# Optimization experiments

Hardware: AMD Instinct MI355X
Metric: run time of the kernel (lower is better)

## Reference

```python
import jax, jax.numpy as jnp
import numpy as np

NUM_EXPERT = 16
IN_FEAT = 1024
OUT_FEAT = 1024
BATCH = 8192


def setup_inputs() -> dict:
    key = jax.random.key(0)
    k_inp, k_gate, k_w = jax.random.split(key, 3)
    inp = jax.random.normal(k_inp, (BATCH, IN_FEAT), dtype=jnp.float32)
    gate = jax.random.randint(k_gate, (BATCH,), 0, NUM_EXPERT, dtype=jnp.int32)
    # nn.Linear default init: uniform(-1/sqrt(in_feat), 1/sqrt(in_feat))
    bound = 1.0 / np.sqrt(IN_FEAT)
    weight = jax.random.uniform(
        k_w, (NUM_EXPERT, OUT_FEAT, IN_FEAT), dtype=jnp.float32,
        minval=-bound, maxval=bound)
    return {"inp": inp, "gate": gate, "weight": weight}


def reference(inp, gate, weight):
    # o[t] = weight[gate[t]] @ inp[t]
    # Loop over the (small, fixed) expert axis via lax.scan; each step does a
    # dense [B, in] @ [in, out] GEMM and keeps rows routed to that expert.
    num_expert, out_feat, _ = weight.shape
    batch = inp.shape[0]

    def body(o, xs):
        i, w = xs  # w: [out_feat, in_feat]
        y = inp @ w.T  # [batch, out_feat]
        sel = (gate == i)[:, None]
        return jnp.where(sel, y, o), None

    o0 = jnp.zeros((batch, out_feat), dtype=inp.dtype)
    o, _ = jax.lax.scan(body, o0, (jnp.arange(num_expert), weight))
    return o
```

## Files before the change

### kernel.cpp

```cpp
#include <hip/hip_runtime.h>
#include <hip/hip_bf16.h>

#define NE    16
#define KDIM  1024
#define NDIM  1024
#define BATCH 8192
#define TM    128
#define TN    64
#define MAXT  96

typedef __attribute__((ext_vector_type(8))) short short8;
typedef __attribute__((ext_vector_type(4))) float floatx4;
typedef unsigned short ushort_t;

#define O_CNT  0
#define O_TG0  256
#define O_TE   1024
#define O_TEND 2048
#define O_POS  4096
#define O_TOK  36864
#define O_PA   73728
#define WS_REQ 17113088

#define GLOAD_LDS(gp, lp) __builtin_amdgcn_global_load_lds( \
    (const __attribute__((address_space(1))) unsigned int*)(gp), \
    (__attribute__((address_space(3))) unsigned int*)(lp), 16, 0, 0)

__device__ __forceinline__ unsigned int pk2bf(float x, float y) {
    __hip_bfloat162 h = __float22bfloat162_rn(make_float2(x, y));
    unsigned int u;
    __builtin_memcpy(&u, &h, 4);
    return u;
}


__global__ void zero_k(int* cnt) {
    if (threadIdx.x < NE) cnt[threadIdx.x] = 0;
}

__global__ void hist_k(const int* __restrict__ gate, int* cnt, int* pos) {
    int t = blockIdx.x * blockDim.x + threadIdx.x;
    if (t < BATCH) pos[t] = atomicAdd(&cnt[gate[t]], 1);
}

__global__ __launch_bounds__(256, 8) void prep_k(
        const float* __restrict__ inp, const int* __restrict__ gate,
        const int* __restrict__ pos, const int* __restrict__ cnt,
        ushort_t* __restrict__ pA, int* __restrict__ tok,
        int* __restrict__ tg0, int* __restrict__ te, int* __restrict__ tend) {
    __shared__ int ntot;
    const int b = blockIdx.x, tid = threadIdx.x;
    if (b < 2048) {
        const int col = (tid & 127) * 8;
        const int half = tid >> 7;
        int g[2]; float4 v0[2], v1[2];
        #pragma unroll
        for (int p = 0; p < 2; ++p) {
            int t = b * 4 + p * 2 + half;
            int e = gate[t];
            int off = 0;
            #pragma unroll
            for (int k = 0; k < NE; ++k) off += (k < e) ? cnt[k] : 0;
            g[p] = off + pos[t];
            v0[p] = *(const float4*)&inp[(size_t)t * KDIM + col];
            v1[p] = *(const float4*)&inp[(size_t)t * KDIM + col + 4];
        }
        #pragma unroll
        for (int p = 0; p < 2; ++p) {
            uint4 u = make_uint4(pk2bf(v0[p].x, v0[p].y), pk2bf(v0[p].z, v0[p].w),
                                 pk2bf(v1[p].x, v1[p].y), pk2bf(v1[p].z, v1[p].w));
            *(uint4*)&pA[(size_t)g[p] * KDIM + col] = u;
            if (col == 0) tok[g[p]] = b * 4 + p * 2 + half;
        }
    } else {
        if (tid < NE) {
            int o = 0, ts = 0;
            for (int j = 0; j < NE; ++j) {
                int c = cnt[j];
                if (j < tid) { o += c; ts += (c + TM - 1) / TM; }
            }
            int c = cnt[tid];
            if (tid == NE - 1) ntot = ts + (c + TM - 1) / TM;
            int nt = ts;
            for (int r = 0; r < c; r += TM) {
                int r0 = (r + TM <= c) ? r : (c > TM ? c - TM : 0);
                tg0[nt] = o + r0; te[nt] = tid; tend[nt] = o + c; ++nt;
            }
        }
        __syncthreads();
        for (int i = ntot + tid; i < MAXT; i += 256) {
            tg0[i] = 0; te[i] = 0; tend[i] = 0;
        }
    }
}

__global__ __launch_bounds__(256, 5) void moe_gemm5_k(
        const ushort_t* __restrict__ pA, const float* __restrict__ wgt,
        const int* __restrict__ tg0, const int* __restrict__ teArr,
        const int* __restrict__ tend, const int* __restrict__ tok,
        float* __restrict__ out) {
    const int y   = blockIdx.y;
    const int g0  = tg0[y];
    const int end = tend[y];
    if (g0 >= end) return;
    const int e    = teArr[y];
    const int out0 = blockIdx.x * TN;

    __shared__ ushort_t As[TM][64];
    __shared__ ushort_t Bs[TN][64];
    __shared__ int tok_s[TM];

    const int tid = threadIdx.x;
    if (tid < TM) tok_s[tid] = tok[g0 + tid];

    const int wave = tid >> 6, lane = tid & 63;
    const int wm = (wave >> 1) * 64;
    const int wn = (wave & 1) * 32;
    const int quad = lane >> 4, l16 = lane & 15;

    const ushort_t* Ab = pA + (size_t)g0 * KDIM;
    const float*    Bw = wgt + ((size_t)e * NDIM + out0) * KDIM;

    floatx4 acc[4][2] = {};
    const int slotw = wave * 64 + lane;

    for (int k0 = 0; k0 < KDIM; k0 += 64) {
        float4 bv[2][2];
        #pragma unroll
        for (int i = 0; i < 2; ++i) {
            int slot = i * 256 + slotw;
            int row = slot >> 3;
            int kc = (slot & 7) ^ (row & 7);
            const float* src = Bw + (size_t)row * KDIM + k0 + kc * 8;
            bv[i][0] = *(const float4*)src;
            bv[i][1] = *(const float4*)(src + 4);
        }
        #pragma unroll
        for (int i = 0; i < 4; ++i) {
            int slot = i * 256 + slotw;
            int row = slot >> 3;
            int kc = (slot & 7) ^ (row & 7);
            GLOAD_LDS(Ab + (size_t)row * KDIM + k0 + kc * 8,
                      (ushort_t*)As + (size_t)(i * 256 + wave * 64) * 8);
        }
        #pragma unroll
        for (int i = 0; i < 2; ++i) {
            int slot = i * 256 + slotw;
            uint4 u = make_uint4(pk2bf(bv[i][0].x, bv[i][0].y),
                                 pk2bf(bv[i][0].z, bv[i][0].w),
                                 pk2bf(bv[i][1].x, bv[i][1].y),
                                 pk2bf(bv[i][1].z, bv[i][1].w));
            *(uint4*)((ushort_t*)Bs + (size_t)slot * 8) = u;
        }
        __syncthreads();
        #pragma unroll
        for (int s = 0; s < 2; ++s) {
            short8 a[4], b[2];
            #pragma unroll
            for (int i = 0; i < 4; ++i) {
                int r = wm + i * 16 + l16;
                a[i] = *(const short8*)&As[r][((s * 4 + quad) ^ (r & 7)) * 8];
            }
            #pragma unroll
            for (int j = 0; j < 2; ++j) {
                int r = wn + j * 16 + l16;
                b[j] = *(const short8*)&Bs[r][((s * 4 + quad) ^ (r & 7)) * 8];
            }
            #pragma unroll
            for (int mi = 0; mi < 4; ++mi)
                #pragma unroll
                for (int nj = 0; nj < 2; ++nj)
                    acc[mi][nj] = __builtin_amdgcn_mfma_f32_16x16x32_bf16(
                        a[mi], b[nj], acc[mi][nj], 0, 0, 0);
        }
        __syncthreads();
    }

    #pragma unroll
    for (int mi = 0; mi < 4; ++mi) {
        #pragma unroll
        for (int r = 0; r < 4; ++r) {
            int lrow = wm + mi * 16 + quad * 4 + r;
            if (g0 + lrow < end) {
                int t = tok_s[lrow];
                float* orow = out + (size_t)t * NDIM + out0 + wn + l16;
                #pragma unroll
                for (int nj = 0; nj < 2; ++nj)
                    orow[nj * 16] = acc[mi][nj][r];
            }
        }
    }
}

#define LDW 20
__global__ void bin_tokens_k(const int* __restrict__ gate, int* cnt, int* idx) {
    int t = blockIdx.x * blockDim.x + threadIdx.x;
    if (t < BATCH) {
        int e = gate[t];
        int p = atomicAdd(&cnt[e], 1);
        idx[e * BATCH + p] = t;
    }
}

__global__ __launch_bounds__(256) void moe_gemm_k(
        const float* __restrict__ inp, const float* __restrict__ wgt,
        const int* __restrict__ cnt, const int* __restrict__ idx,
        float* __restrict__ out) {
    const int e = blockIdx.z;
    const int n_e = cnt[e];
    const int row0 = blockIdx.y * TM;
    if (row0 >= n_e) return;
    const int out0 = blockIdx.x * 128;
    __shared__ unsigned int As[TM * LDW];
    __shared__ unsigned int Bs[TM * LDW];
    __shared__ int tok_s[TM];
    const int tid = threadIdx.x;
    if (tid < TM) {
        int g = row0 + tid;
        tok_s[tid] = (g < n_e) ? idx[e * BATCH + g] : -1;
    }
    const int wave = tid >> 6, lane = tid & 63;
    const int wm = (wave >> 1) * 64, wn = (wave & 1) * 64;
    const int quad = lane >> 4, l16 = lane & 15;
    floatx4 acc[4][4] = {};
    const int cg = (tid & 7) * 4;
    const int rbase = tid >> 3;
    const float* wbase = wgt + (size_t)e * KDIM * NDIM;
    for (int k0 = 0; k0 < KDIM; k0 += 32) {
        __syncthreads();
        #pragma unroll
        for (int p = 0; p < 4; ++p) {
            int row = p * 32 + rbase;
            int t = tok_s[row];
            float4 va = make_float4(0.f, 0.f, 0.f, 0.f);
            if (t >= 0) va = *(const float4*)&inp[(size_t)t * KDIM + k0 + cg];
            As[row * LDW + (cg >> 1)]     = pk2bf(va.x, va.y);
            As[row * LDW + (cg >> 1) + 1] = pk2bf(va.z, va.w);
            float4 vb = *(const float4*)&wbase[(size_t)(out0 + row) * KDIM + k0 + cg];
            Bs[row * LDW + (cg >> 1)]     = pk2bf(vb.x, vb.y);
            Bs[row * LDW + (cg >> 1) + 1] = pk2bf(vb.z, vb.w);
        }
        __syncthreads();
        short8 a[4], b[4];
        #pragma unroll
        for (int i = 0; i < 4; ++i)
            a[i] = *(const short8*)&As[(wm + i * 16 + l16) * LDW + quad * 4];
        #pragma unroll
        for (int i = 0; i < 4; ++i)
            b[i] = *(const short8*)&Bs[(wn + i * 16 + l16) * LDW + quad * 4];
        #pragma unroll
        for (int mi = 0; mi < 4; ++mi)
            #pragma unroll
            for (int ni = 0; ni < 4; ++ni)
                acc[mi][ni] = __builtin_amdgcn_mfma_f32_16x16x32_bf16(
                    a[mi], b[ni], acc[mi][ni], 0, 0, 0);
    }
    #pragma unroll
    for (int mi = 0; mi < 4; ++mi) {
        #pragma unroll
        for (int r = 0; r < 4; ++r) {
            int lrow = wm + mi * 16 + quad * 4 + r;
            int t = tok_s[lrow];
            if (t >= 0) {
                float* orow = out + (size_t)t * NDIM + out0 + wn + l16;
                #pragma unroll
                for (int ni = 0; ni < 4; ++ni)
                    orow[ni * 16] = acc[mi][ni][r];
            }
        }
    }
}

extern "C" void kernel_launch(void* const* d_in, const int* in_sizes, int n_in,
                              void* d_out, int out_size, void* d_ws, size_t ws_size,
                              hipStream_t stream) {
    const float* inp  = (const float*)d_in[0];
    const int*   gate = (const int*)d_in[1];
    const float* wgt  = (const float*)d_in[2];
    float*       out  = (float*)d_out;
    char* w = (char*)d_ws;

    if (ws_size >= WS_REQ) {
        int* cnt  = (int*)(w + O_CNT);
        int* tg0  = (int*)(w + O_TG0);
        int* te   = (int*)(w + O_TE);
        int* tend = (int*)(w + O_TEND);
        int* pos  = (int*)(w + O_POS);
        int* tok  = (int*)(w + O_TOK);
        ushort_t* pA = (ushort_t*)(w + O_PA);

        zero_k<<<1, 64, 0, stream>>>(cnt);
        hist_k<<<BATCH / 256, 256, 0, stream>>>(gate, cnt, pos);
        prep_k<<<2048 + 1, 256, 0, stream>>>(inp, gate, pos, cnt,
                                             pA, tok, tg0, te, tend);
        dim3 grid(NDIM / TN, MAXT, 1);
        moe_gemm5_k<<<grid, 256, 0, stream>>>(pA, wgt, tg0, te, tend, tok, out);
    } else {
        int* cnt = (int*)d_ws;
        int* idx = cnt + NE;
        zero_k<<<1, 64, 0, stream>>>(cnt);
        bin_tokens_k<<<BATCH / 256, 256, 0, stream>>>(gate, cnt, idx);
        dim3 grid(NDIM / 128, BATCH / TM, NE);
        moe_gemm_k<<<grid, 256, 0, stream>>>(inp, wgt, cnt, idx, out);
    }
}
```

Measured before the change: 192.7 us.

## Double-buffer A tile with register-prefetched B and block-local histogram

The GEMM kernel now keeps two A tiles in LDS and prefetches the next K-step's weights into registers and the next A tile via global_load_lds while the MFMAs for the current step run. The trailing __syncthreads becomes an lgkmcnt wait plus a raw barrier. Occupancy hint drops from 5 to 4 blocks. The histogram now aggregates per block in shared memory before a single global atomic per expert, with counters padded to separate cache lines. The risks are more LDS and register pressure, and the raw barrier may not wait for the outstanding async A loads (vmcnt), which could race.

```diff
diff --git a/kernel.cpp b/kernel.cpp
--- a/kernel.cpp
+++ b/kernel.cpp
@@ -8,15 +8,16 @@
 #define TM    128
 #define TN    64
 #define MAXT  96
+#define CSTR  16
 
 typedef __attribute__((ext_vector_type(8))) short short8;
 typedef __attribute__((ext_vector_type(4))) float floatx4;
 typedef unsigned short ushort_t;
 
 #define O_CNT  0
-#define O_TG0  256
-#define O_TE   1024
-#define O_TEND 2048
+#define O_TG0  1024
+#define O_TE   2048
+#define O_TEND 3072
 #define O_POS  4096
 #define O_TOK  36864
 #define O_PA   73728
@@ -35,12 +36,23 @@
 
 
 __global__ void zero_k(int* cnt) {
-    if (threadIdx.x < NE) cnt[threadIdx.x] = 0;
-}
-
-__global__ void hist_k(const int* __restrict__ gate, int* cnt, int* pos) {
-    int t = blockIdx.x * blockDim.x + threadIdx.x;
-    if (t < BATCH) pos[t] = atomicAdd(&cnt[gate[t]], 1);
+    if (threadIdx.x < NE * CSTR) cnt[threadIdx.x] = 0;
+}
+
+__global__ __launch_bounds__(256) void hist_k(
+        const int* __restrict__ gate, int* cnt, int* pos) {
+    __shared__ int lc[NE];
+    __shared__ int lb[NE];
+    const int tid = threadIdx.x;
+    if (tid < NE) lc[tid] = 0;
+    __syncthreads();
+    const int t = blockIdx.x * 256 + tid;
+    const int e = gate[t];
+    const int r = atomicAdd(&lc[e], 1);
+    __syncthreads();
+    if (tid < NE) lb[tid] = atomicAdd(&cnt[tid * CSTR], lc[tid]);
+    __syncthreads();
+    pos[t] = lb[e] + r;
 }
 
 __global__ __launch_bounds__(256, 8) void prep_k(
@@ -60,7 +72,7 @@
             int e = gate[t];
             int off = 0;
             #pragma unroll
-            for (int k = 0; k < NE; ++k) off += (k < e) ? cnt[k] : 0;
+            for (int k = 0; k < NE; ++k) off += (k < e) ? cnt[k * CSTR] : 0;
             g[p] = off + pos[t];
             v0[p] = *(const float4*)&inp[(size_t)t * KDIM + col];
             v1[p] = *(const float4*)&inp[(size_t)t * KDIM + col + 4];
@@ -76,10 +88,10 @@
         if (tid < NE) {
             int o = 0, ts = 0;
             for (int j = 0; j < NE; ++j) {
-                int c = cnt[j];
+                int c = cnt[j * CSTR];
                 if (j < tid) { o += c; ts += (c + TM - 1) / TM; }
             }
-            int c = cnt[tid];
+            int c = cnt[tid * CSTR];
             if (tid == NE - 1) ntot = ts + (c + TM - 1) / TM;
             int nt = ts;
             for (int r = 0; r < c; r += TM) {
@@ -94,7 +106,7 @@
     }
 }
 
-__global__ __launch_bounds__(256, 5) void moe_gemm5_k(
+__global__ __launch_bounds__(256, 4) void moe_gemm5_k(
         const ushort_t* __restrict__ pA, const float* __restrict__ wgt,
         const int* __restrict__ tg0, const int* __restrict__ teArr,
         const int* __restrict__ tend, const int* __restrict__ tok,
@@ -106,43 +118,42 @@
     const int e    = teArr[y];
     const int out0 = blockIdx.x * TN;
 
-    __shared__ ushort_t As[TM][64];
+    __shared__ ushort_t As[2][TM][64];
     __shared__ ushort_t Bs[TN][64];
-    __shared__ int tok_s[TM];
 
     const int tid = threadIdx.x;
-    if (tid < TM) tok_s[tid] = tok[g0 + tid];
-
     const int wave = tid >> 6, lane = tid & 63;
     const int wm = (wave >> 1) * 64;
     const int wn = (wave & 1) * 32;
     const int quad = lane >> 4, l16 = lane & 15;
+    const int slotw = wave * 64 + lane;
 
     const ushort_t* Ab = pA + (size_t)g0 * KDIM;
     const float*    Bw = wgt + ((size_t)e * NDIM + out0) * KDIM;
 
     floatx4 acc[4][2] = {};
-    const int slotw = wave * 64 + lane;
-
+    float4 bv[2][2];
+
+    #pragma unroll
+    for (int i = 0; i < 2; ++i) {
+        int slot = i * 256 + slotw;
+        int row = slot >> 3;
+        int kc = (slot & 7) ^ (row & 7);
+        const float* src = Bw + (size_t)row * KDIM + kc * 8;
+        bv[i][0] = *(const float4*)src;
+        bv[i][1] = *(const float4*)(src + 4);
+    }
+    #pragma unroll
+    for (int i = 0; i < 4; ++i) {
+        int slot = i * 256 + slotw;
+        int row = slot >> 3;
+        int kc = (slot & 7) ^ (row & 7);
+        GLOAD_LDS(Ab + (size_t)row * KDIM + kc * 8,
+                  (ushort_t*)As[0] + (size_t)(i * 256 + wave * 64) * 8);
+    }
+
+    int cur = 0;
     for (int k0 = 0; k0 < KDIM; k0 += 64) {
-        float4 bv[2][2];
-        #pragma unroll
-        for (int i = 0; i < 2; ++i) {
-            int slot = i * 256 + slotw;
-            int row = slot >> 3;
-            int kc = (slot & 7) ^ (row & 7);
-            const float* src = Bw + (size_t)row * KDIM + k0 + kc * 8;
-            bv[i][0] = *(const float4*)src;
-            bv[i][1] = *(const float4*)(src + 4);
-        }
-        #pragma unroll
-        for (int i = 0; i < 4; ++i) {
-            int slot = i * 256 + slotw;
-            int row = slot >> 3;
-            int kc = (slot & 7) ^ (row & 7);
-            GLOAD_LDS(Ab + (size_t)row * KDIM + k0 + kc * 8,
-                      (ushort_t*)As + (size_t)(i * 256 + wave * 64) * 8);
-        }
         #pragma unroll
         for (int i = 0; i < 2; ++i) {
             int slot = i * 256 + slotw;
@@ -153,13 +164,34 @@
             *(uint4*)((ushort_t*)Bs + (size_t)slot * 8) = u;
         }
         __syncthreads();
+
+        if (k0 + 64 < KDIM) {
+            #pragma unroll
+            for (int i = 0; i < 2; ++i) {
+                int slot = i * 256 + slotw;
+                int row = slot >> 3;
+                int kc = (slot & 7) ^ (row & 7);
+                const float* src = Bw + (size_t)row * KDIM + (k0 + 64) + kc * 8;
+                bv[i][0] = *(const float4*)src;
+                bv[i][1] = *(const float4*)(src + 4);
+            }
+            #pragma unroll
+            for (int i = 0; i < 4; ++i) {
+                int slot = i * 256 + slotw;
+                int row = slot >> 3;
+                int kc = (slot & 7) ^ (row & 7);
+                GLOAD_LDS(Ab + (size_t)row * KDIM + (k0 + 64) + kc * 8,
+                          (ushort_t*)As[cur ^ 1] + (size_t)(i * 256 + wave * 64) * 8);
+            }
+        }
+
         #pragma unroll
         for (int s = 0; s < 2; ++s) {
             short8 a[4], b[2];
             #pragma unroll
             for (int i = 0; i < 4; ++i) {
                 int r = wm + i * 16 + l16;
-                a[i] = *(const short8*)&As[r][((s * 4 + quad) ^ (r & 7)) * 8];
+                a[i] = *(const short8*)&As[cur][r][((s * 4 + quad) ^ (r & 7)) * 8];
             }
             #pragma unroll
             for (int j = 0; j < 2; ++j) {
@@ -173,7 +205,9 @@
                     acc[mi][nj] = __builtin_amdgcn_mfma_f32_16x16x32_bf16(
                         a[mi], b[nj], acc[mi][nj], 0, 0, 0);
         }
-        __syncthreads();
+        asm volatile("s_waitcnt lgkmcnt(0)" ::: "memory");
+        __builtin_amdgcn_s_barrier();
+        cur ^= 1;
     }
 
     #pragma unroll
@@ -182,7 +216,7 @@
         for (int r = 0; r < 4; ++r) {
             int lrow = wm + mi * 16 + quad * 4 + r;
             if (g0 + lrow < end) {
-                int t = tok_s[lrow];
+                int t = tok[g0 + lrow];
                 float* orow = out + (size_t)t * NDIM + out0 + wn + l16;
                 #pragma unroll
                 for (int nj = 0; nj < 2; ++nj)
@@ -289,7 +323,7 @@
         int* tok  = (int*)(w + O_TOK);
         ushort_t* pA = (ushort_t*)(w + O_PA);
 
-        zero_k<<<1, 64, 0, stream>>>(cnt);
+        zero_k<<<1, 256, 0, stream>>>(cnt);
         hist_k<<<BATCH / 256, 256, 0, stream>>>(gate, cnt, pos);
         prep_k<<<2048 + 1, 256, 0, stream>>>(inp, gate, pos, cnt,
                                              pA, tok, tg0, te, tend);
```

Result: faster. 181.7 us (-5.7%).
